# Kernel tuning notes

Measured on AMD Instinct MI355X. Metric: run time of the kernel, lower is better.

## Reference

```python
import jax, jax.numpy as jnp
import numpy as np

L, D, H, KV, HD, KVL, I, PL = 8, 2048, 8, 2, 256, 4096, 8192, 256
FULL = (4,)          # layers with full (global) attention / global RoPE
POS = 2047           # current decode position (cache write slot)
N_REP = H // KV      # GQA expansion factor


def rms(x, eps=1e-6):
    # RMSNorm without scale (v_norm); scale applied by caller where needed
    return x * jax.lax.rsqrt(jnp.mean(x * x, axis=-1, keepdims=True) + eps)


def rope(x, cos, sin):
    half = HD // 2
    rot = jnp.concatenate([-x[..., half:], x[..., :half]], axis=-1)
    return x * cos + rot * sin


def _rope_tables(theta):
    inv = 1.0 / (theta ** (np.arange(0, HD, 2, dtype=np.float32) / HD))
    ang = jnp.asarray(POS * inv, dtype=jnp.float32)
    return jnp.concatenate([jnp.cos(ang)] * 2), jnp.concatenate([jnp.sin(ang)] * 2)


def setup_inputs() -> dict:
    key = jax.random.key(0)
    ks = jax.random.split(key, 24)
    r = lambda k, s, sc=0.02: jax.random.normal(k, s, jnp.float32) * sc
    gains = lambda k, s: 1.0 + jax.random.normal(k, s, jnp.float32) * 0.02
    cos_s, sin_s = _rope_tables(10000.0)
    cos_f, sin_f = _rope_tables(1000000.0)
    um = jnp.zeros((1, 1, KVL, 1), jnp.float32).at[0, 0, POS, 0].set(1.0)
    mask = jnp.where(jnp.arange(KVL) <= POS, 0.0, -1e9).astype(jnp.float32)
    return {
        "hidden_states": r(ks[0], (1, 1, D), 1.0),
        "causal_mask": mask,
        "update_mask": um,
        "per_layer_combined": r(ks[1], (1, 1, L * PL), 1.0),
        "cos_s": cos_s, "sin_s": sin_s, "cos_f": cos_f, "sin_f": sin_f,
        "K_in": r(ks[2], (L, KV, KVL, HD)),
        "V_in": r(ks[3], (L, KV, KVL, HD)),
        "w_q": r(ks[4], (L, H * HD, D)),
        "w_k": r(ks[5], (L, KV * HD, D)),
        "w_v": r(ks[6], (L, KV * HD, D)),
        "w_o": r(ks[7], (L, D, H * HD)),
        "g_in_ln": gains(ks[8], (L, D)),
        "g_q_norm": gains(ks[9], (L, HD)),
        "g_k_norm": gains(ks[10], (L, HD)),
        "g_post_attn_ln": gains(ks[11], (L, D)),
        "g_pre_ff_ln": gains(ks[12], (L, D)),
        "g_post_ff_ln": gains(ks[13], (L, D)),
        "w_gate": r(ks[14], (L, I, D)),
        "w_up": r(ks[15], (L, I, D)),
        "w_down": r(ks[16], (L, D, I)),
        "w_plg": r(ks[17], (L, PL, D)),
        "w_plp": r(ks[18], (L, D, PL)),
        "g_post_pl_ln": gains(ks[19], (L, D)),
        "layer_scalar": jnp.ones((L,), jnp.float32),
    }


def reference(hidden_states, causal_mask, update_mask, per_layer_combined,
              cos_s, sin_s, cos_f, sin_f, K_in, V_in,
              w_q, w_k, w_v, w_o,
              g_in_ln, g_q_norm, g_k_norm, g_post_attn_ln, g_pre_ff_ln, g_post_ff_ln,
              w_gate, w_up, w_down, w_plg, w_plp, g_post_pl_ln, layer_scalar):
    um = update_mask[0, 0]          # [KVL,1] one-hot at write position
    h = hidden_states[0, 0]         # [D], batch=1/seq=1 decode
    K_outs, V_outs = [], []
    for i in range(L):
        cos, sin = (cos_f, sin_f) if i in FULL else (cos_s, sin_s)
        # --- attention block ---
        res = h
        x = rms(h) * g_in_ln[i]
        q = rms((w_q[i] @ x).reshape(H, HD)) * g_q_norm[i]
        q = rope(q, cos, sin)                                   # [H,HD]
        k = rms((w_k[i] @ x).reshape(KV, HD)) * g_k_norm[i]
        k = rope(k, cos, sin)                                   # [KV,HD]
        v = rms((w_v[i] @ x).reshape(KV, HD))                    # v_norm (no scale)
        # full-tensor masked blend = KV cache write (faithful to source)
        Ko = K_in[i] * (1.0 - um) + k[:, None, :] * um          # [KV,KVL,HD]
        Vo = V_in[i] * (1.0 - um) + v[:, None, :] * um
        K_outs.append(Ko); V_outs.append(Vo)
        Ke = jnp.repeat(Ko, N_REP, axis=0)                      # GQA expand [H,KVL,HD]
        Ve = jnp.repeat(Vo, N_REP, axis=0)
        scores = jnp.einsum('hd,hkd->hk', q, Ke) + causal_mask  # no 1/sqrt(hd) in source
        attn = jax.nn.softmax(scores, axis=-1)
        ao = jnp.einsum('hk,hkd->hd', attn, Ve).reshape(H * HD)
        ao = rms(w_o[i] @ ao) * g_post_attn_ln[i]
        h = res + ao
        # --- gated MLP ---
        res = h
        xm = rms(h) * g_pre_ff_ln[i]
        m = w_down[i] @ (jax.nn.gelu(w_gate[i] @ xm, approximate=True) * (w_up[i] @ xm))
        h = res + rms(m) * g_post_ff_ln[i]
        # --- per-layer input gating ---
        res = h
        pls = per_layer_combined[0, 0, i * PL:(i + 1) * PL]     # [PL]
        g = jax.nn.gelu(w_plg[i] @ h, approximate=True) * pls
        h = res + rms(w_plp[i] @ g) * g_post_pl_ln[i]
        h = h * layer_scalar[i]
    return (h[None, None, :], jnp.stack(K_outs), jnp.stack(V_outs))
```

## Files before the change

kernel.cpp:

```cpp
#include <hip/hip_runtime.h>

#define NL   8
#define DIM  2048
#define NH   8
#define NKV  2
#define HD   256
#define KVL  4096
#define FFI  8192
#define PLD  256
#define POS  2047
#define NCH  128
#define CP   16

__device__ __forceinline__ float dot4(float4 a, float4 b){
  return a.x*b.x + a.y*b.y + a.z*b.z + a.w*b.w;
}

__device__ __forceinline__ float waveAllSum(float v){
#pragma unroll
  for(int o=1;o<64;o<<=1) v += __shfl_xor(v,o,64);
  return v;
}

__device__ __forceinline__ float blockSum256(float v, float* red){
  int lane = threadIdx.x & 63, w = threadIdx.x >> 6;
  v = waveAllSum(v);
  __syncthreads();
  if(lane==0) red[w] = v;
  __syncthreads();
  return red[0]+red[1]+red[2]+red[3];
}

__device__ __forceinline__ float gelu_tanh(float v){
  return 0.5f*v*(1.0f + tanhf(0.7978845608028654f*(v + 0.044715f*v*v*v)));
}

__device__ __forceinline__ float4 normRope(const float* __restrict__ raw, int lane,
    const float* __restrict__ gain, const float* __restrict__ cosT,
    const float* __restrict__ sinT, bool doRope){
  float4 v4 = ((const float4*)raw)[lane];
  float ss = waveAllSum(dot4(v4,v4));
  float sc = rsqrtf(ss*(1.f/HD) + 1e-6f);
  float4 n;
  if(gain){
    float4 g4 = ((const float4*)gain)[lane];
    n.x=v4.x*sc*g4.x; n.y=v4.y*sc*g4.y; n.z=v4.z*sc*g4.z; n.w=v4.w*sc*g4.w;
  } else {
    n.x=v4.x*sc; n.y=v4.y*sc; n.z=v4.z*sc; n.w=v4.w*sc;
  }
  if(!doRope) return n;
  float4 np;
  np.x=__shfl_xor(n.x,32,64); np.y=__shfl_xor(n.y,32,64);
  np.z=__shfl_xor(n.z,32,64); np.w=__shfl_xor(n.w,32,64);
  float4 c4 = ((const float4*)cosT)[lane];
  float4 s4 = ((const float4*)sinT)[lane];
  float sg = (lane < 32) ? -1.f : 1.f;
  float4 o;
  o.x = n.x*c4.x + sg*np.x*s4.x;
  o.y = n.y*c4.y + sg*np.y*s4.y;
  o.z = n.z*c4.z + sg*np.z*s4.z;
  o.w = n.w*c4.w + sg*np.w*s4.w;
  return o;
}

__global__ __launch_bounds__(256) void qkv_k(
    const float* __restrict__ Wq, const float* __restrict__ Wk,
    const float* __restrict__ Wv,
    const float* __restrict__ hC, const float* __restrict__ u,
    const float* __restrict__ g_pl, const float* __restrict__ lsc,
    const float* __restrict__ g_in, const float* __restrict__ hidden,
    float* __restrict__ hA, float* __restrict__ qkv){
  __shared__ float xs[DIM];
  __shared__ float red[4];
  int tid = threadIdx.x;
  float hv[8];
  if(hidden){
#pragma unroll
    for(int i=0;i<8;i++) hv[i] = hidden[tid + i*256];
  } else {
    float uv[8]; float ss1 = 0.f;
#pragma unroll
    for(int i=0;i<8;i++){ uv[i] = u[tid + i*256]; ss1 += uv[i]*uv[i]; }
    ss1 = blockSum256(ss1, red);
    float r1 = rsqrtf(ss1*(1.f/DIM) + 1e-6f);
    float ls = lsc[0];
#pragma unroll
    for(int i=0;i<8;i++){
      int idx = tid + i*256;
      hv[i] = (hC[idx] + uv[i]*r1*g_pl[idx])*ls;
    }
  }
  float ss2 = 0.f;
#pragma unroll
  for(int i=0;i<8;i++) ss2 += hv[i]*hv[i];
  ss2 = blockSum256(ss2, red);
  float r2 = rsqrtf(ss2*(1.f/DIM) + 1e-6f);
#pragma unroll
  for(int i=0;i<8;i++){
    int idx = tid + i*256;
    xs[idx] = hv[i]*r2*g_in[idx];
    if(blockIdx.x==0) hA[idx] = hv[i];
  }
  __syncthreads();
  int lane = tid & 63, wv = tid >> 6;
  int r = blockIdx.x*4 + wv;
  const float* W; int row;
  if(r < 2048){ W = Wq; row = r; }
  else if(r < 2560){ W = Wk; row = r - 2048; }
  else { W = Wv; row = r - 2560; }
  const float4* Wr = (const float4*)(W + (size_t)row*DIM);
  const float4* xs4 = (const float4*)xs;
  float4 w8[8];
#pragma unroll
  for(int i=0;i<8;i++) w8[i] = Wr[i*64+lane];
  float acc = 0.f;
#pragma unroll
  for(int i=0;i<8;i++) acc += dot4(w8[i], xs4[i*64+lane]);
  acc = waveAllSum(acc);
  if(lane==0) qkv[r] = acc;
}

__global__ __launch_bounds__(256) void attn_k(
    const float* __restrict__ qkvb,
    const float* __restrict__ gq, const float* __restrict__ gk,
    const float* __restrict__ cosT, const float* __restrict__ sinT,
    float* __restrict__ Kl, float* __restrict__ Vl,
    float* __restrict__ pm, float* __restrict__ pl, float* __restrict__ po){
  int b = blockIdx.x, tid = threadIdx.x, lane = tid & 63, wv = tid >> 6;

  if(b == NKV*NCH){
    int kvv = wv >> 1, isV = wv & 1;
    const float* raw = qkvb + (isV ? 2560 : 2048) + kvv*HD;
    float4 o = normRope(raw, lane, isV ? nullptr : gk, cosT, sinT, !isV);
    float* dst = (isV ? Vl : Kl) + ((size_t)kvv*KVL + POS)*HD;
    ((float4*)dst)[lane] = o;
    return;
  }

  int kv = b & 1, c = b >> 1;
  __shared__ float q_s[4][HD];
  __shared__ float vf_s[HD];
  __shared__ float s_s[4][CP];
  __shared__ float s_w[4][CP];
  bool fresh = (c == NCH-1);

  {
    float4 o = normRope(qkvb + (kv*4 + wv)*HD, lane, gq, cosT, sinT, true);
    ((float4*)q_s[wv])[lane] = o;
  }
  float4 kf4 = {0,0,0,0};
  if(fresh){
    if(wv == 3) kf4 = normRope(qkvb + 2048 + kv*HD, lane, gk, cosT, sinT, true);
    if(wv == 1){
      float4 o = normRope(qkvb + 2560 + kv*HD, lane, nullptr, cosT, sinT, false);
      ((float4*)vf_s)[lane] = o;
    }
  }
  __syncthreads();

  float4 q4[4];
#pragma unroll
  for(int hh=0;hh<4;hh++) q4[hh] = ((const float4*)q_s[hh])[lane];
  const float4* Kp = (const float4*)(Kl + ((size_t)kv*KVL + c*CP)*HD);
#pragma unroll
  for(int j=0;j<4;j++){
    int p = wv*4 + j;
    float4 k4 = (fresh && p==CP-1) ? kf4 : Kp[(size_t)p*64 + lane];
    float d0 = dot4(k4,q4[0]), d1 = dot4(k4,q4[1]);
    float d2 = dot4(k4,q4[2]), d3 = dot4(k4,q4[3]);
    d0 = waveAllSum(d0); d1 = waveAllSum(d1);
    d2 = waveAllSum(d2); d3 = waveAllSum(d3);
    if(lane==0){ s_s[0][p]=d0; s_s[1][p]=d1; s_s[2][p]=d2; s_s[3][p]=d3; }
  }
  __syncthreads();

  if(tid < 64){
    int hh = tid >> 4, pp = tid & 15;
    float s = s_s[hh][pp];
    float m = s;
#pragma unroll
    for(int o=1;o<16;o<<=1) m = fmaxf(m, __shfl_xor(m,o,64));
    float e = __expf(s - m);
    float ls = e;
#pragma unroll
    for(int o=1;o<16;o<<=1) ls += __shfl_xor(ls,o,64);
    s_w[hh][pp] = e;
    if(pp==0){ int hg = kv*4 + hh; pm[hg*NCH + c] = m; pl[hg*NCH + c] = ls; }
  }
  __syncthreads();

  int d = tid;
  const float* Vp = Vl + ((size_t)kv*KVL + c*CP)*HD;
  float vv[CP];
#pragma unroll
  for(int p2=0;p2<CP;p2++) vv[p2] = Vp[(size_t)p2*HD + d];
  if(fresh) vv[CP-1] = vf_s[d];
  float acc[4] = {0.f,0.f,0.f,0.f};
#pragma unroll
  for(int p2=0;p2<CP;p2++){
#pragma unroll
    for(int hh=0;hh<4;hh++) acc[hh] += s_w[hh][p2]*vv[p2];
  }
#pragma unroll
  for(int hh=0;hh<4;hh++)
    po[((size_t)(kv*4+hh)*NCH + c)*HD + d] = acc[hh];
}

__global__ __launch_bounds__(256) void attn_c(const float* __restrict__ pm,
    const float* __restrict__ pl, const float* __restrict__ po, float* __restrict__ ao){
  int h = blockIdx.x, tid = threadIdx.x;
  __shared__ float sm[NCH], sl[NCH], se[NCH];
  if(tid < NCH){ sm[tid] = pm[h*NCH+tid]; sl[tid] = pl[h*NCH+tid]; }
  __syncthreads();
  float M = -1e30f;
  for(int c=0;c<NCH;c++) M = fmaxf(M, sm[c]);
  if(tid < NCH) se[tid] = __expf(sm[tid]-M);
  __syncthreads();
  float Lh = 0.f;
  for(int c=0;c<NCH;c++) Lh += sl[c]*se[c];
  float a0=0.f, a1=0.f, a2=0.f, a3=0.f;
#pragma unroll 1
  for(int c=0;c<NCH;c+=4){
    a0 += po[((size_t)h*NCH + c  )*HD + tid]*se[c];
    a1 += po[((size_t)h*NCH + c+1)*HD + tid]*se[c+1];
    a2 += po[((size_t)h*NCH + c+2)*HD + tid]*se[c+2];
    a3 += po[((size_t)h*NCH + c+3)*HD + tid]*se[c+3];
  }
  ao[h*HD + tid] = (a0+a1+a2+a3) / Lh;
}

template<int C>
__global__ __launch_bounds__(256) void gemv_k(const float* __restrict__ W,
    const float* __restrict__ x, float* __restrict__ y){
  __shared__ float xs[C];
  for(int i=threadIdx.x; i<C/4; i+=256)
    ((float4*)xs)[i] = ((const float4*)x)[i];
  __syncthreads();
  int lane = threadIdx.x & 63, wv = threadIdx.x >> 6;
  int r = blockIdx.x*4 + wv;
  const float4* Wr = (const float4*)(W + (size_t)r*C);
  const float4* xs4 = (const float4*)xs;
  float acc = 0.f;
#pragma unroll
  for(int ii=0;ii<C/2048;ii++){
    float4 w8[8];
#pragma unroll
    for(int i=0;i<8 && ii*8+i < C/256;i++) w8[i] = Wr[(ii*8+i)*64+lane];
#pragma unroll
    for(int i=0;i<8 && ii*8+i < C/256;i++) acc += dot4(w8[i], xs4[(ii*8+i)*64+lane]);
  }
  if(C < 2048){
    float4 w1 = Wr[lane];
    acc = dot4(w1, xs4[lane]);
  }
  acc = waveAllSum(acc);
  if(lane==0) y[r] = acc;
}

__global__ __launch_bounds__(256) void gateup_k(const float* __restrict__ Wg,
    const float* __restrict__ Wu, const float* __restrict__ y,
    const float* __restrict__ hA, const float* __restrict__ g_pa,
    const float* __restrict__ g_pf, float* __restrict__ hB, float* __restrict__ t){
  __shared__ float xs[DIM];
  __shared__ float red[4];
  int tid = threadIdx.x;
  float yv[8]; float ss1 = 0.f;
#pragma unroll
  for(int i=0;i<8;i++){ yv[i] = y[tid + i*256]; ss1 += yv[i]*yv[i]; }
  ss1 = blockSum256(ss1, red);
  float r1 = rsqrtf(ss1*(1.f/DIM) + 1e-6f);
  float hv[8]; float ss2 = 0.f;
#pragma unroll
  for(int i=0;i<8;i++){
    int idx = tid + i*256;
    hv[i] = hA[idx] + yv[i]*r1*g_pa[idx];
    ss2 += hv[i]*hv[i];
  }
  ss2 = blockSum256(ss2, red);
  float r2 = rsqrtf(ss2*(1.f/DIM) + 1e-6f);
#pragma unroll
  for(int i=0;i<8;i++){
    int idx = tid + i*256;
    xs[idx] = hv[i]*r2*g_pf[idx];
    if(blockIdx.x==0) hB[idx] = hv[i];
  }
  __syncthreads();
  int lane = tid & 63, wv = tid >> 6;
  int j = blockIdx.x*4 + wv;
  const float4* Gr = (const float4*)(Wg + (size_t)j*DIM);
  const float4* Ur = (const float4*)(Wu + (size_t)j*DIM);
  const float4* xs4 = (const float4*)xs;
  float4 g8[8], u8[8];
#pragma unroll
  for(int i=0;i<8;i++) g8[i] = Gr[i*64+lane];
#pragma unroll
  for(int i=0;i<8;i++) u8[i] = Ur[i*64+lane];
  float ag = 0.f, au = 0.f;
#pragma unroll
  for(int i=0;i<8;i++){
    float4 bv = xs4[i*64+lane];
    ag += dot4(g8[i], bv);
    au += dot4(u8[i], bv);
  }
  ag = waveAllSum(ag);
  au = waveAllSum(au);
  if(lane==0) t[j] = gelu_tanh(ag)*au;
}

__global__ __launch_bounds__(256) void down_k(const float* __restrict__ Wd,
    const float* __restrict__ t, float* __restrict__ mv){
  __shared__ float red[4];
  int tid = threadIdx.x, lane = tid & 63, wv = tid >> 6;
  int r = blockIdx.x;
  const float4* Wr = (const float4*)(Wd + (size_t)r*FFI) + wv*512;
  const float4* tp = (const float4*)t + wv*512;
  float4 w8[8], t8[8];
#pragma unroll
  for(int i=0;i<8;i++) w8[i] = Wr[i*64+lane];
#pragma unroll
  for(int i=0;i<8;i++) t8[i] = tp[i*64+lane];
  float acc = 0.f;
#pragma unroll
  for(int i=0;i<8;i++) acc += dot4(w8[i], t8[i]);
  acc = waveAllSum(acc);
  if(lane==0) red[wv] = acc;
  __syncthreads();
  if(tid==0) mv[r] = red[0]+red[1]+red[2]+red[3];
}

__global__ __launch_bounds__(256) void plg_k(const float* __restrict__ W,
    const float* __restrict__ mv, const float* __restrict__ hB,
    const float* __restrict__ g_ff, const float* __restrict__ pls,
    float* __restrict__ hCout, float* __restrict__ gb){
  __shared__ float xs[DIM];
  __shared__ float red[4];
  int tid = threadIdx.x;
  float mvv[8]; float ss1 = 0.f;
#pragma unroll
  for(int i=0;i<8;i++){ mvv[i] = mv[tid + i*256]; ss1 += mvv[i]*mvv[i]; }
  ss1 = blockSum256(ss1, red);
  float r1 = rsqrtf(ss1*(1.f/DIM) + 1e-6f);
#pragma unroll
  for(int i=0;i<8;i++){
    int idx = tid + i*256;
    float hc = hB[idx] + mvv[i]*r1*g_ff[idx];
    xs[idx] = hc;
    if(blockIdx.x==0) hCout[idx] = hc;
  }
  __syncthreads();
  int lane = tid & 63, wv = tid >> 6;
  int r = blockIdx.x*4 + wv;
  const float4* Wr = (const float4*)(W + (size_t)r*DIM);
  const float4* xs4 = (const float4*)xs;
  float4 w8[8];
#pragma unroll
  for(int i=0;i<8;i++) w8[i] = Wr[i*64+lane];
  float acc = 0.f;
#pragma unroll
  for(int i=0;i<8;i++) acc += dot4(w8[i], xs4[i*64+lane]);
  acc = waveAllSum(acc);
  if(lane==0) gb[r] = gelu_tanh(acc)*pls[r];
}

__global__ __launch_bounds__(256) void final_k(const float* __restrict__ u,
    const float* __restrict__ hC, const float* __restrict__ g_pl,
    const float* __restrict__ lsc, float* __restrict__ out){
  __shared__ float red[4];
  int tid = threadIdx.x;
  float uv[8]; float ss1 = 0.f;
#pragma unroll
  for(int i=0;i<8;i++){ uv[i] = u[tid + i*256]; ss1 += uv[i]*uv[i]; }
  ss1 = blockSum256(ss1, red);
  float r1 = rsqrtf(ss1*(1.f/DIM) + 1e-6f);
  float ls = lsc[0];
#pragma unroll
  for(int i=0;i<8;i++){
    int idx = tid + i*256;
    out[idx] = (hC[idx] + uv[i]*r1*g_pl[idx])*ls;
  }
}

extern "C" void kernel_launch(void* const* d_in, const int* in_sizes, int n_in,
                              void* d_out, int out_size, void* d_ws, size_t ws_size,
                              hipStream_t stream){
  const float* hidden   = (const float*)d_in[0];
  const float* plc      = (const float*)d_in[3];
  const float* cos_s    = (const float*)d_in[4];
  const float* sin_s    = (const float*)d_in[5];
  const float* cos_f    = (const float*)d_in[6];
  const float* sin_f    = (const float*)d_in[7];
  const float* K_in     = (const float*)d_in[8];
  const float* V_in     = (const float*)d_in[9];
  const float* w_q      = (const float*)d_in[10];
  const float* w_k      = (const float*)d_in[11];
  const float* w_v      = (const float*)d_in[12];
  const float* w_o      = (const float*)d_in[13];
  const float* g_in_ln  = (const float*)d_in[14];
  const float* g_q_norm = (const float*)d_in[15];
  const float* g_k_norm = (const float*)d_in[16];
  const float* g_pa_ln  = (const float*)d_in[17];
  const float* g_pf_ln  = (const float*)d_in[18];
  const float* g_ff_ln  = (const float*)d_in[19];
  const float* w_gate   = (const float*)d_in[20];
  const float* w_up     = (const float*)d_in[21];
  const float* w_down   = (const float*)d_in[22];
  const float* w_plg    = (const float*)d_in[23];
  const float* w_plp    = (const float*)d_in[24];
  const float* g_pl_ln  = (const float*)d_in[25];
  const float* l_scal   = (const float*)d_in[26];

  float* out  = (float*)d_out;
  float* outK = out + DIM;
  float* outV = outK + (size_t)NL*NKV*KVL*HD;

  float* ws   = (float*)d_ws;
  float* hA   = ws;
  float* hB   = ws + 2048;
  float* hC   = ws + 4096;
  float* qkvb = ws + 6144;
  float* y    = ws + 9216;
  float* t    = ws + 11264;
  float* mv   = ws + 19456;
  float* gb   = ws + 21504;
  float* u    = ws + 21760;
  float* pm   = ws + 23808;
  float* pl   = ws + 24832;
  float* po   = ws + 25856;
  float* ao   = ws + 288000;

  (void)hipMemcpyAsync(outK, K_in, (size_t)NL*NKV*KVL*HD*sizeof(float),
                       hipMemcpyDeviceToDevice, stream);
  (void)hipMemcpyAsync(outV, V_in, (size_t)NL*NKV*KVL*HD*sizeof(float),
                       hipMemcpyDeviceToDevice, stream);

  for(int l=0;l<NL;l++){
    const float* cosT = (l==4) ? cos_f : cos_s;
    const float* sinT = (l==4) ? sin_f : sin_s;
    float* Kl = outK + (size_t)l*NKV*KVL*HD;
    float* Vl = outV + (size_t)l*NKV*KVL*HD;

    qkv_k<<<768,256,0,stream>>>(
        w_q + (size_t)l*NH*HD*DIM, w_k + (size_t)l*NKV*HD*DIM,
        w_v + (size_t)l*NKV*HD*DIM,
        hC, u,
        (l>0) ? g_pl_ln + (size_t)(l-1)*DIM : g_pl_ln,
        (l>0) ? l_scal + (l-1) : l_scal,
        g_in_ln + (size_t)l*DIM,
        (l==0) ? hidden : nullptr,
        hA, qkvb);

    attn_k<<<NKV*NCH+1,256,0,stream>>>(qkvb, g_q_norm + l*HD, g_k_norm + l*HD,
                                       cosT, sinT, Kl, Vl, pm, pl, po);

    attn_c<<<NH,256,0,stream>>>(pm, pl, po, ao);

    gemv_k<DIM><<<512,256,0,stream>>>(w_o + (size_t)l*DIM*NH*HD, ao, y);

    gateup_k<<<FFI/4,256,0,stream>>>(w_gate + (size_t)l*FFI*DIM,
                                     w_up + (size_t)l*FFI*DIM,
                                     y, hA, g_pa_ln + (size_t)l*DIM,
                                     g_pf_ln + (size_t)l*DIM, hB, t);

    down_k<<<DIM,256,0,stream>>>(w_down + (size_t)l*DIM*FFI, t, mv);

    plg_k<<<PLD/4,256,0,stream>>>(w_plg + (size_t)l*PLD*DIM, mv, hB,
                                  g_ff_ln + (size_t)l*DIM, plc + l*PLD, hC, gb);

    gemv_k<PLD><<<512,256,0,stream>>>(w_plp + (size_t)l*DIM*PLD, gb, u);
  }

  final_k<<<1,256,0,stream>>>(u, hC, g_pl_ln + (size_t)(NL-1)*DIM,
                              l_scal + (NL-1), out);
}
```

Before: 809.2 us.

## Fuse per-layer kernels into two persistent kernels with atomic-counter stage handoff

Replaces the eight launches per layer with two kernels. Within each kernel, block ranges act as pipeline stages that signal completion and wait on one another through global atomic counters with release and acquire fences. The bulk K/V cache copy moves off the separate memcpy calls and into spare blocks of the attention kernel, using nontemporal loads and stores so it can overlap with compute. Attention now reads the old cache directly from the inputs. The aim is to cut launch gaps and to hide the large cache copy. The cost is reliance on lower-index blocks being scheduled before the blocks that wait on them, which risks deadlock or spin overhead if they are not.

```diff
diff --git a/kernel.cpp b/kernel.cpp
--- a/kernel.cpp
+++ b/kernel.cpp
@@ -12,8 +12,19 @@
 #define NCH  128
 #define CP   16
 
+typedef float vfloat4 __attribute__((ext_vector_type(4)));
+
 __device__ __forceinline__ float dot4(float4 a, float4 b){
   return a.x*b.x + a.y*b.y + a.z*b.z + a.w*b.w;
+}
+
+__device__ __forceinline__ float4 ntld4(const float4* p){
+  vfloat4 v = __builtin_nontemporal_load((const vfloat4*)p);
+  float4 r; r.x=v.x; r.y=v.y; r.z=v.z; r.w=v.w; return r;
+}
+__device__ __forceinline__ void ntst4(float4* p, float4 v){
+  vfloat4 t; t.x=v.x; t.y=v.y; t.z=v.z; t.w=v.w;
+  __builtin_nontemporal_store(t, (vfloat4*)p);
 }
 
 __device__ __forceinline__ float waveAllSum(float v){
@@ -63,320 +74,367 @@
   return o;
 }
 
-__global__ __launch_bounds__(256) void qkv_k(
-    const float* __restrict__ Wq, const float* __restrict__ Wk,
-    const float* __restrict__ Wv,
-    const float* __restrict__ hC, const float* __restrict__ u,
-    const float* __restrict__ g_pl, const float* __restrict__ lsc,
-    const float* __restrict__ g_in, const float* __restrict__ hidden,
-    float* __restrict__ hA, float* __restrict__ qkv){
-  __shared__ float xs[DIM];
+__device__ __forceinline__ void prodSignal(unsigned* c){
+  __syncthreads();
+  if(threadIdx.x == 0){
+    __builtin_amdgcn_fence(__ATOMIC_RELEASE, "agent");
+    __hip_atomic_fetch_add(c, 1u, __ATOMIC_RELAXED, __HIP_MEMORY_SCOPE_AGENT);
+  }
+}
+__device__ __forceinline__ void consWait(unsigned* c, unsigned n){
+  if(threadIdx.x == 0){
+    while(__hip_atomic_load(c, __ATOMIC_RELAXED, __HIP_MEMORY_SCOPE_AGENT) < n)
+      __builtin_amdgcn_s_sleep(2);
+    __builtin_amdgcn_fence(__ATOMIC_ACQUIRE, "agent");
+  }
+  __syncthreads();
+}
+
+__global__ __launch_bounds__(256,4) void init_k(const float* __restrict__ hidden,
+    const float* __restrict__ gin, float* __restrict__ hRes, float* __restrict__ xs){
   __shared__ float red[4];
   int tid = threadIdx.x;
-  float hv[8];
-  if(hidden){
-#pragma unroll
-    for(int i=0;i<8;i++) hv[i] = hidden[tid + i*256];
+  float v[8]; float ss = 0.f;
+#pragma unroll
+  for(int i=0;i<8;i++){ v[i] = hidden[tid + i*256]; ss += v[i]*v[i]; }
+  ss = blockSum256(ss, red);
+  float r = rsqrtf(ss*(1.f/DIM) + 1e-6f);
+#pragma unroll
+  for(int i=0;i<8;i++){ int idx = tid + i*256; hRes[idx] = v[i]; xs[idx] = v[i]*r*gin[idx]; }
+}
+
+__global__ __launch_bounds__(256,4) void ab_k(
+    const float* __restrict__ Wq, const float* __restrict__ Wk,
+    const float* __restrict__ Wv, const float* __restrict__ Wo,
+    const float* __restrict__ Ki, const float* __restrict__ Vi,
+    float* __restrict__ Kl, float* __restrict__ Vl,
+    const float* __restrict__ gq, const float* __restrict__ gk,
+    const float* __restrict__ cosT, const float* __restrict__ sinT,
+    const float* __restrict__ xs, float* __restrict__ qkvb,
+    float* __restrict__ pm, float* __restrict__ pl, float* __restrict__ po,
+    float* __restrict__ ao, float* __restrict__ y,
+    const float* __restrict__ hRes, const float* __restrict__ gpa,
+    const float* __restrict__ gpf, float* __restrict__ hMid, float* __restrict__ xm,
+    unsigned* cnt){
+  __shared__ float sh[2048];
+  __shared__ float red[4];
+  float4* sh4 = (float4*)sh;
+  int b = blockIdx.x, tid = threadIdx.x, lane = tid & 63, wv = tid >> 6;
+  unsigned* c_qkv  = cnt;
+  unsigned* c_attn = cnt + 16;
+  unsigned* c_comb = cnt + 32;
+  unsigned* c_wo   = cnt + 48;
+
+  if(b < 384){
+#pragma unroll
+    for(int i=0;i<2;i++) sh4[tid + i*256] = ((const float4*)xs)[tid + i*256];
+    __syncthreads();
+#pragma unroll
+    for(int rr=0;rr<2;rr++){
+      int r = b*8 + wv*2 + rr;
+      const float* W; int row;
+      if(r < 2048){ W = Wq; row = r; }
+      else if(r < 2560){ W = Wk; row = r - 2048; }
+      else { W = Wv; row = r - 2560; }
+      const float4* Wr = (const float4*)(W + (size_t)row*DIM);
+      float4 w8[8];
+#pragma unroll
+      for(int i=0;i<8;i++) w8[i] = Wr[i*64+lane];
+      float acc = 0.f;
+#pragma unroll
+      for(int i=0;i<8;i++) acc += dot4(w8[i], sh4[i*64+lane]);
+      acc = waveAllSum(acc);
+      if(lane==0) qkvb[r] = acc;
+    }
+    prodSignal(c_qkv);
+  } else if(b < 641){
+    consWait(c_qkv, 384);
+    int b2 = b - 384;
+    if(b2 == 256){
+      int kvv = wv >> 1, isV = wv & 1;
+      const float* raw = qkvb + (isV ? 2560 : 2048) + kvv*HD;
+      float4 o = normRope(raw, lane, isV ? nullptr : gk, cosT, sinT, !isV);
+      float* dst = (isV ? Vl : Kl) + ((size_t)kvv*KVL + POS)*HD;
+      ((float4*)dst)[lane] = o;
+      prodSignal(c_attn);
+      return;
+    }
+    int kv = b2 & 1, c = b2 >> 1;
+    float* q_s  = sh;
+    float* vf_s = sh + 1024;
+    float* s_sB = sh + 1280;
+    float* s_wB = sh + 1344;
+    bool fresh = (c == NCH-1);
+    { float4 o = normRope(qkvb + (kv*4 + wv)*HD, lane, gq, cosT, sinT, true);
+      ((float4*)(q_s + wv*HD))[lane] = o; }
+    float4 kf4 = {0,0,0,0};
+    if(fresh){
+      if(wv == 3) kf4 = normRope(qkvb + 2048 + kv*HD, lane, gk, cosT, sinT, true);
+      if(wv == 1){
+        float4 o = normRope(qkvb + 2560 + kv*HD, lane, nullptr, cosT, sinT, false);
+        ((float4*)vf_s)[lane] = o;
+      }
+    }
+    __syncthreads();
+    float4 q4[4];
+#pragma unroll
+    for(int hh=0;hh<4;hh++) q4[hh] = ((const float4*)(q_s + hh*HD))[lane];
+    const float4* Kp = (const float4*)(Ki + ((size_t)kv*KVL + c*CP)*HD);
+#pragma unroll
+    for(int j=0;j<4;j++){
+      int p = wv*4 + j;
+      float4 k4 = (fresh && p==CP-1) ? kf4 : Kp[(size_t)p*64 + lane];
+      float d0 = dot4(k4,q4[0]), d1 = dot4(k4,q4[1]);
+      float d2 = dot4(k4,q4[2]), d3 = dot4(k4,q4[3]);
+      d0 = waveAllSum(d0); d1 = waveAllSum(d1);
+      d2 = waveAllSum(d2); d3 = waveAllSum(d3);
+      if(lane==0){ s_sB[0*CP+p]=d0; s_sB[1*CP+p]=d1; s_sB[2*CP+p]=d2; s_sB[3*CP+p]=d3; }
+    }
+    __syncthreads();
+    if(tid < 64){
+      int hh = tid >> 4, pp = tid & 15;
+      float s = s_sB[hh*CP+pp];
+      float m = s;
+#pragma unroll
+      for(int o=1;o<16;o<<=1) m = fmaxf(m, __shfl_xor(m,o,64));
+      float e = __expf(s - m);
+      float ls = e;
+#pragma unroll
+      for(int o=1;o<16;o<<=1) ls += __shfl_xor(ls,o,64);
+      s_wB[hh*CP+pp] = e;
+      if(pp==0){ int hg = kv*4 + hh; pm[hg*NCH + c] = m; pl[hg*NCH + c] = ls; }
+    }
+    __syncthreads();
+    int d = tid;
+    const float* Vp = Vi + ((size_t)kv*KVL + c*CP)*HD;
+    float vv[CP];
+#pragma unroll
+    for(int p2=0;p2<CP;p2++) vv[p2] = Vp[(size_t)p2*HD + d];
+    if(fresh) vv[CP-1] = vf_s[d];
+    float acc[4] = {0.f,0.f,0.f,0.f};
+#pragma unroll
+    for(int p2=0;p2<CP;p2++){
+#pragma unroll
+      for(int hh=0;hh<4;hh++) acc[hh] += s_wB[hh*CP+p2]*vv[p2];
+    }
+#pragma unroll
+    for(int hh=0;hh<4;hh++)
+      po[((size_t)(kv*4+hh)*NCH + c)*HD + d] = acc[hh];
+    prodSignal(c_attn);
+  } else if(b < 649){
+    consWait(c_attn, 257);
+    int h = b - 641;
+    float* sm = sh; float* sl = sh + 128; float* se = sh + 256;
+    if(tid < NCH){ sm[tid] = pm[h*NCH+tid]; sl[tid] = pl[h*NCH+tid]; }
+    __syncthreads();
+    float M = -1e30f;
+    for(int c=0;c<NCH;c++) M = fmaxf(M, sm[c]);
+    if(tid < NCH) se[tid] = __expf(sm[tid]-M);
+    __syncthreads();
+    float Lh = 0.f;
+    for(int c=0;c<NCH;c++) Lh += sl[c]*se[c];
+    float a0=0.f,a1=0.f,a2=0.f,a3=0.f;
+#pragma unroll 1
+    for(int c=0;c<NCH;c+=4){
+      a0 += po[((size_t)h*NCH + c  )*HD + tid]*se[c];
+      a1 += po[((size_t)h*NCH + c+1)*HD + tid]*se[c+1];
+      a2 += po[((size_t)h*NCH + c+2)*HD + tid]*se[c+2];
+      a3 += po[((size_t)h*NCH + c+3)*HD + tid]*se[c+3];
+    }
+    ao[h*HD + tid] = (a0+a1+a2+a3) / Lh;
+    prodSignal(c_comb);
+  } else if(b < 777){
+    consWait(c_comb, 8);
+    int b4 = b - 649;
+#pragma unroll
+    for(int i=0;i<2;i++) sh4[tid + i*256] = ((const float4*)ao)[tid + i*256];
+    __syncthreads();
+#pragma unroll
+    for(int j=0;j<4;j++){
+      int r = b4*16 + wv*4 + j;
+      const float4* Wr = (const float4*)(Wo + (size_t)r*DIM);
+      float4 w8[8];
+#pragma unroll
+      for(int i=0;i<8;i++) w8[i] = Wr[i*64+lane];
+      float acc = 0.f;
+#pragma unroll
+      for(int i=0;i<8;i++) acc += dot4(w8[i], sh4[i*64+lane]);
+      acc = waveAllSum(acc);
+      if(lane==0) y[r] = acc;
+    }
+    prodSignal(c_wo);
+  } else if(b == 777){
+    consWait(c_wo, 128);
+    float yv[8]; float ss1 = 0.f;
+#pragma unroll
+    for(int i=0;i<8;i++){ yv[i] = y[tid + i*256]; ss1 += yv[i]*yv[i]; }
+    ss1 = blockSum256(ss1, red);
+    float r1 = rsqrtf(ss1*(1.f/DIM) + 1e-6f);
+    float hv[8]; float ss2 = 0.f;
+#pragma unroll
+    for(int i=0;i<8;i++){
+      int idx = tid + i*256;
+      hv[i] = hRes[idx] + yv[i]*r1*gpa[idx];
+      ss2 += hv[i]*hv[i];
+    }
+    ss2 = blockSum256(ss2, red);
+    float r2 = rsqrtf(ss2*(1.f/DIM) + 1e-6f);
+#pragma unroll
+    for(int i=0;i<8;i++){
+      int idx = tid + i*256;
+      hMid[idx] = hv[i];
+      xm[idx] = hv[i]*r2*gpf[idx];
+    }
   } else {
+    int b5 = b - 778;
+#pragma unroll 4
+    for(int i=0;i<32;i++){
+      int gr = b5*128 + wv*32 + i;
+      int pos = gr & 4095;
+      if(pos == POS) continue;
+      const float4* s; float4* dpt;
+      if(gr < 8192){ s = (const float4*)Ki + (size_t)gr*64; dpt = (float4*)Kl + (size_t)gr*64; }
+      else { int g2 = gr - 8192; s = (const float4*)Vi + (size_t)g2*64; dpt = (float4*)Vl + (size_t)g2*64; }
+      ntst4(dpt + lane, ntld4(s + lane));
+    }
+  }
+}
+
+__global__ __launch_bounds__(256,4) void cde_k(
+    const float* __restrict__ Wg, const float* __restrict__ Wu,
+    const float* __restrict__ Wd, const float* __restrict__ Wpg,
+    const float* __restrict__ Wpp,
+    const float* __restrict__ xm, float* __restrict__ t, float* __restrict__ mv,
+    const float* __restrict__ hMid, const float* __restrict__ gff,
+    const float* __restrict__ pls, float* __restrict__ hFF, float* __restrict__ gb,
+    float* __restrict__ u,
+    const float* __restrict__ gpl, const float* __restrict__ lsc,
+    const float* __restrict__ ginN, float* __restrict__ hRes, float* __restrict__ xs,
+    float* __restrict__ outv,
+    unsigned* cnt){
+  __shared__ float sh[8192];
+  __shared__ float red[4];
+  float4* sh4 = (float4*)sh;
+  int b = blockIdx.x, tid = threadIdx.x, lane = tid & 63, wv = tid >> 6;
+  unsigned* c_gu   = cnt + 64;
+  unsigned* c_down = cnt + 80;
+  unsigned* c_plg  = cnt + 96;
+  unsigned* c_plp  = cnt + 112;
+
+  if(b < 256){
+#pragma unroll
+    for(int i=0;i<2;i++) sh4[tid + i*256] = ((const float4*)xm)[tid + i*256];
+    __syncthreads();
+#pragma unroll 1
+    for(int jj=0;jj<8;jj++){
+      int j = b*32 + wv*8 + jj;
+      const float4* Gr = (const float4*)(Wg + (size_t)j*DIM);
+      const float4* Ur = (const float4*)(Wu + (size_t)j*DIM);
+      float4 g8[8], u8[8];
+#pragma unroll
+      for(int i=0;i<8;i++) g8[i] = Gr[i*64+lane];
+#pragma unroll
+      for(int i=0;i<8;i++) u8[i] = Ur[i*64+lane];
+      float ag = 0.f, au = 0.f;
+#pragma unroll
+      for(int i=0;i<8;i++){
+        float4 bv = sh4[i*64+lane];
+        ag += dot4(g8[i], bv);
+        au += dot4(u8[i], bv);
+      }
+      ag = waveAllSum(ag);
+      au = waveAllSum(au);
+      if(lane==0) t[j] = gelu_tanh(ag)*au;
+    }
+    prodSignal(c_gu);
+  } else if(b < 768){
+    consWait(c_gu, 256);
+#pragma unroll
+    for(int i=0;i<8;i++) sh4[tid + i*256] = ((const float4*)t)[tid + i*256];
+    __syncthreads();
+    int r = (b-256)*4 + wv;
+    const float4* Wr = (const float4*)(Wd + (size_t)r*FFI);
+    float acc = 0.f;
+#pragma unroll 1
+    for(int bb=0;bb<4;bb++){
+      float4 w8[8];
+#pragma unroll
+      for(int i=0;i<8;i++) w8[i] = Wr[(bb*8+i)*64+lane];
+#pragma unroll
+      for(int i=0;i<8;i++) acc += dot4(w8[i], sh4[(bb*8+i)*64+lane]);
+    }
+    acc = waveAllSum(acc);
+    if(lane==0) mv[r] = acc;
+    prodSignal(c_down);
+  } else if(b < 832){
+    consWait(c_down, 512);
+    float mvv[8]; float ss1 = 0.f;
+#pragma unroll
+    for(int i=0;i<8;i++){ mvv[i] = mv[tid + i*256]; ss1 += mvv[i]*mvv[i]; }
+    ss1 = blockSum256(ss1, red);
+    float r1 = rsqrtf(ss1*(1.f/DIM) + 1e-6f);
+#pragma unroll
+    for(int i=0;i<8;i++){
+      int idx = tid + i*256;
+      float hc = hMid[idx] + mvv[i]*r1*gff[idx];
+      sh[idx] = hc;
+      if(b==768) hFF[idx] = hc;
+    }
+    __syncthreads();
+    int r = (b-768)*4 + wv;
+    const float4* Wr = (const float4*)(Wpg + (size_t)r*DIM);
+    float4 w8[8];
+#pragma unroll
+    for(int i=0;i<8;i++) w8[i] = Wr[i*64+lane];
+    float acc = 0.f;
+#pragma unroll
+    for(int i=0;i<8;i++) acc += dot4(w8[i], sh4[i*64+lane]);
+    acc = waveAllSum(acc);
+    if(lane==0) gb[r] = gelu_tanh(acc)*pls[r];
+    prodSignal(c_plg);
+  } else if(b < 960){
+    consWait(c_plg, 64);
+    if(tid < 64) sh4[tid] = ((const float4*)gb)[tid];
+    __syncthreads();
+#pragma unroll
+    for(int j=0;j<4;j++){
+      int r = (b-832)*16 + wv*4 + j;
+      const float4* Wr = (const float4*)(Wpp + (size_t)r*PLD);
+      float acc = dot4(Wr[lane], sh4[lane]);
+      acc = waveAllSum(acc);
+      if(lane==0) u[r] = acc;
+    }
+    prodSignal(c_plp);
+  } else {
+    consWait(c_plp, 128);
     float uv[8]; float ss1 = 0.f;
 #pragma unroll
     for(int i=0;i<8;i++){ uv[i] = u[tid + i*256]; ss1 += uv[i]*uv[i]; }
     ss1 = blockSum256(ss1, red);
     float r1 = rsqrtf(ss1*(1.f/DIM) + 1e-6f);
     float ls = lsc[0];
+    float h3[8];
 #pragma unroll
     for(int i=0;i<8;i++){
       int idx = tid + i*256;
-      hv[i] = (hC[idx] + uv[i]*r1*g_pl[idx])*ls;
-    }
-  }
-  float ss2 = 0.f;
-#pragma unroll
-  for(int i=0;i<8;i++) ss2 += hv[i]*hv[i];
-  ss2 = blockSum256(ss2, red);
-  float r2 = rsqrtf(ss2*(1.f/DIM) + 1e-6f);
-#pragma unroll
-  for(int i=0;i<8;i++){
-    int idx = tid + i*256;
-    xs[idx] = hv[i]*r2*g_in[idx];
-    if(blockIdx.x==0) hA[idx] = hv[i];
-  }
-  __syncthreads();
-  int lane = tid & 63, wv = tid >> 6;
-  int r = blockIdx.x*4 + wv;
-  const float* W; int row;
-  if(r < 2048){ W = Wq; row = r; }
-  else if(r < 2560){ W = Wk; row = r - 2048; }
-  else { W = Wv; row = r - 2560; }
-  const float4* Wr = (const float4*)(W + (size_t)row*DIM);
-  const float4* xs4 = (const float4*)xs;
-  float4 w8[8];
-#pragma unroll
-  for(int i=0;i<8;i++) w8[i] = Wr[i*64+lane];
-  float acc = 0.f;
-#pragma unroll
-  for(int i=0;i<8;i++) acc += dot4(w8[i], xs4[i*64+lane]);
-  acc = waveAllSum(acc);
-  if(lane==0) qkv[r] = acc;
-}
-
-__global__ __launch_bounds__(256) void attn_k(
-    const float* __restrict__ qkvb,
-    const float* __restrict__ gq, const float* __restrict__ gk,
-    const float* __restrict__ cosT, const float* __restrict__ sinT,
-    float* __restrict__ Kl, float* __restrict__ Vl,
-    float* __restrict__ pm, float* __restrict__ pl, float* __restrict__ po){
-  int b = blockIdx.x, tid = threadIdx.x, lane = tid & 63, wv = tid >> 6;
-
-  if(b == NKV*NCH){
-    int kvv = wv >> 1, isV = wv & 1;
-    const float* raw = qkvb + (isV ? 2560 : 2048) + kvv*HD;
-    float4 o = normRope(raw, lane, isV ? nullptr : gk, cosT, sinT, !isV);
-    float* dst = (isV ? Vl : Kl) + ((size_t)kvv*KVL + POS)*HD;
-    ((float4*)dst)[lane] = o;
-    return;
-  }
-
-  int kv = b & 1, c = b >> 1;
-  __shared__ float q_s[4][HD];
-  __shared__ float vf_s[HD];
-  __shared__ float s_s[4][CP];
-  __shared__ float s_w[4][CP];
-  bool fresh = (c == NCH-1);
-
-  {
-    float4 o = normRope(qkvb + (kv*4 + wv)*HD, lane, gq, cosT, sinT, true);
-    ((float4*)q_s[wv])[lane] = o;
-  }
-  float4 kf4 = {0,0,0,0};
-  if(fresh){
-    if(wv == 3) kf4 = normRope(qkvb + 2048 + kv*HD, lane, gk, cosT, sinT, true);
-    if(wv == 1){
-      float4 o = normRope(qkvb + 2560 + kv*HD, lane, nullptr, cosT, sinT, false);
-      ((float4*)vf_s)[lane] = o;
-    }
-  }
-  __syncthreads();
-
-  float4 q4[4];
-#pragma unroll
-  for(int hh=0;hh<4;hh++) q4[hh] = ((const float4*)q_s[hh])[lane];
-  const float4* Kp = (const float4*)(Kl + ((size_t)kv*KVL + c*CP)*HD);
-#pragma unroll
-  for(int j=0;j<4;j++){
-    int p = wv*4 + j;
-    float4 k4 = (fresh && p==CP-1) ? kf4 : Kp[(size_t)p*64 + lane];
-    float d0 = dot4(k4,q4[0]), d1 = dot4(k4,q4[1]);
-    float d2 = dot4(k4,q4[2]), d3 = dot4(k4,q4[3]);
-    d0 = waveAllSum(d0); d1 = waveAllSum(d1);
-    d2 = waveAllSum(d2); d3 = waveAllSum(d3);
-    if(lane==0){ s_s[0][p]=d0; s_s[1][p]=d1; s_s[2][p]=d2; s_s[3][p]=d3; }
-  }
-  __syncthreads();
-
-  if(tid < 64){
-    int hh = tid >> 4, pp = tid & 15;
-    float s = s_s[hh][pp];
-    float m = s;
-#pragma unroll
-    for(int o=1;o<16;o<<=1) m = fmaxf(m, __shfl_xor(m,o,64));
-    float e = __expf(s - m);
-    float ls = e;
-#pragma unroll
-    for(int o=1;o<16;o<<=1) ls += __shfl_xor(ls,o,64);
-    s_w[hh][pp] = e;
-    if(pp==0){ int hg = kv*4 + hh; pm[hg*NCH + c] = m; pl[hg*NCH + c] = ls; }
-  }
-  __syncthreads();
-
-  int d = tid;
-  const float* Vp = Vl + ((size_t)kv*KVL + c*CP)*HD;
-  float vv[CP];
-#pragma unroll
-  for(int p2=0;p2<CP;p2++) vv[p2] = Vp[(size_t)p2*HD + d];
-  if(fresh) vv[CP-1] = vf_s[d];
-  float acc[4] = {0.f,0.f,0.f,0.f};
-#pragma unroll
-  for(int p2=0;p2<CP;p2++){
-#pragma unroll
-    for(int hh=0;hh<4;hh++) acc[hh] += s_w[hh][p2]*vv[p2];
-  }
-#pragma unroll
-  for(int hh=0;hh<4;hh++)
-    po[((size_t)(kv*4+hh)*NCH + c)*HD + d] = acc[hh];
-}
-
-__global__ __launch_bounds__(256) void attn_c(const float* __restrict__ pm,
-    const float* __restrict__ pl, const float* __restrict__ po, float* __restrict__ ao){
-  int h = blockIdx.x, tid = threadIdx.x;
-  __shared__ float sm[NCH], sl[NCH], se[NCH];
-  if(tid < NCH){ sm[tid] = pm[h*NCH+tid]; sl[tid] = pl[h*NCH+tid]; }
-  __syncthreads();
-  float M = -1e30f;
-  for(int c=0;c<NCH;c++) M = fmaxf(M, sm[c]);
-  if(tid < NCH) se[tid] = __expf(sm[tid]-M);
-  __syncthreads();
-  float Lh = 0.f;
-  for(int c=0;c<NCH;c++) Lh += sl[c]*se[c];
-  float a0=0.f, a1=0.f, a2=0.f, a3=0.f;
-#pragma unroll 1
-  for(int c=0;c<NCH;c+=4){
-    a0 += po[((size_t)h*NCH + c  )*HD + tid]*se[c];
-    a1 += po[((size_t)h*NCH + c+1)*HD + tid]*se[c+1];
-    a2 += po[((size_t)h*NCH + c+2)*HD + tid]*se[c+2];
-    a3 += po[((size_t)h*NCH + c+3)*HD + tid]*se[c+3];
-  }
-  ao[h*HD + tid] = (a0+a1+a2+a3) / Lh;
-}
-
-template<int C>
-__global__ __launch_bounds__(256) void gemv_k(const float* __restrict__ W,
-    const float* __restrict__ x, float* __restrict__ y){
-  __shared__ float xs[C];
-  for(int i=threadIdx.x; i<C/4; i+=256)
-    ((float4*)xs)[i] = ((const float4*)x)[i];
-  __syncthreads();
-  int lane = threadIdx.x & 63, wv = threadIdx.x >> 6;
-  int r = blockIdx.x*4 + wv;
-  const float4* Wr = (const float4*)(W + (size_t)r*C);
-  const float4* xs4 = (const float4*)xs;
-  float acc = 0.f;
-#pragma unroll
-  for(int ii=0;ii<C/2048;ii++){
-    float4 w8[8];
-#pragma unroll
-    for(int i=0;i<8 && ii*8+i < C/256;i++) w8[i] = Wr[(ii*8+i)*64+lane];
-#pragma unroll
-    for(int i=0;i<8 && ii*8+i < C/256;i++) acc += dot4(w8[i], xs4[(ii*8+i)*64+lane]);
-  }
-  if(C < 2048){
-    float4 w1 = Wr[lane];
-    acc = dot4(w1, xs4[lane]);
-  }
-  acc = waveAllSum(acc);
-  if(lane==0) y[r] = acc;
-}
-
-__global__ __launch_bounds__(256) void gateup_k(const float* __restrict__ Wg,
-    const float* __restrict__ Wu, const float* __restrict__ y,
-    const float* __restrict__ hA, const float* __restrict__ g_pa,
-    const float* __restrict__ g_pf, float* __restrict__ hB, float* __restrict__ t){
-  __shared__ float xs[DIM];
-  __shared__ float red[4];
-  int tid = threadIdx.x;
-  float yv[8]; float ss1 = 0.f;
-#pragma unroll
-  for(int i=0;i<8;i++){ yv[i] = y[tid + i*256]; ss1 += yv[i]*yv[i]; }
-  ss1 = blockSum256(ss1, red);
-  float r1 = rsqrtf(ss1*(1.f/DIM) + 1e-6f);
-  float hv[8]; float ss2 = 0.f;
-#pragma unroll
-  for(int i=0;i<8;i++){
-    int idx = tid + i*256;
-    hv[i] = hA[idx] + yv[i]*r1*g_pa[idx];
-    ss2 += hv[i]*hv[i];
-  }
-  ss2 = blockSum256(ss2, red);
-  float r2 = rsqrtf(ss2*(1.f/DIM) + 1e-6f);
-#pragma unroll
-  for(int i=0;i<8;i++){
-    int idx = tid + i*256;
-    xs[idx] = hv[i]*r2*g_pf[idx];
-    if(blockIdx.x==0) hB[idx] = hv[i];
-  }
-  __syncthreads();
-  int lane = tid & 63, wv = tid >> 6;
-  int j = blockIdx.x*4 + wv;
-  const float4* Gr = (const float4*)(Wg + (size_t)j*DIM);
-  const float4* Ur = (const float4*)(Wu + (size_t)j*DIM);
-  const float4* xs4 = (const float4*)xs;
-  float4 g8[8], u8[8];
-#pragma unroll
-  for(int i=0;i<8;i++) g8[i] = Gr[i*64+lane];
-#pragma unroll
-  for(int i=0;i<8;i++) u8[i] = Ur[i*64+lane];
-  float ag = 0.f, au = 0.f;
-#pragma unroll
-  for(int i=0;i<8;i++){
-    float4 bv = xs4[i*64+lane];
-    ag += dot4(g8[i], bv);
-    au += dot4(u8[i], bv);
-  }
-  ag = waveAllSum(ag);
-  au = waveAllSum(au);
-  if(lane==0) t[j] = gelu_tanh(ag)*au;
-}
-
-__global__ __launch_bounds__(256) void down_k(const float* __restrict__ Wd,
-    const float* __restrict__ t, float* __restrict__ mv){
-  __shared__ float red[4];
-  int tid = threadIdx.x, lane = tid & 63, wv = tid >> 6;
-  int r = blockIdx.x;
-  const float4* Wr = (const float4*)(Wd + (size_t)r*FFI) + wv*512;
-  const float4* tp = (const float4*)t + wv*512;
-  float4 w8[8], t8[8];
-#pragma unroll
-  for(int i=0;i<8;i++) w8[i] = Wr[i*64+lane];
-#pragma unroll
-  for(int i=0;i<8;i++) t8[i] = tp[i*64+lane];
-  float acc = 0.f;
-#pragma unroll
-  for(int i=0;i<8;i++) acc += dot4(w8[i], t8[i]);
-  acc = waveAllSum(acc);
-  if(lane==0) red[wv] = acc;
-  __syncthreads();
-  if(tid==0) mv[r] = red[0]+red[1]+red[2]+red[3];
-}
-
-__global__ __launch_bounds__(256) void plg_k(const float* __restrict__ W,
-    const float* __restrict__ mv, const float* __restrict__ hB,
-    const float* __restrict__ g_ff, const float* __restrict__ pls,
-    float* __restrict__ hCout, float* __restrict__ gb){
-  __shared__ float xs[DIM];
-  __shared__ float red[4];
-  int tid = threadIdx.x;
-  float mvv[8]; float ss1 = 0.f;
-#pragma unroll
-  for(int i=0;i<8;i++){ mvv[i] = mv[tid + i*256]; ss1 += mvv[i]*mvv[i]; }
-  ss1 = blockSum256(ss1, red);
-  float r1 = rsqrtf(ss1*(1.f/DIM) + 1e-6f);
-#pragma unroll
-  for(int i=0;i<8;i++){
-    int idx = tid + i*256;
-    float hc = hB[idx] + mvv[i]*r1*g_ff[idx];
-    xs[idx] = hc;
-    if(blockIdx.x==0) hCout[idx] = hc;
-  }
-  __syncthreads();
-  int lane = tid & 63, wv = tid >> 6;
-  int r = blockIdx.x*4 + wv;
-  const float4* Wr = (const float4*)(W + (size_t)r*DIM);
-  const float4* xs4 = (const float4*)xs;
-  float4 w8[8];
-#pragma unroll
-  for(int i=0;i<8;i++) w8[i] = Wr[i*64+lane];
-  float acc = 0.f;
-#pragma unroll
-  for(int i=0;i<8;i++) acc += dot4(w8[i], xs4[i*64+lane]);
-  acc = waveAllSum(acc);
-  if(lane==0) gb[r] = gelu_tanh(acc)*pls[r];
-}
-
-__global__ __launch_bounds__(256) void final_k(const float* __restrict__ u,
-    const float* __restrict__ hC, const float* __restrict__ g_pl,
-    const float* __restrict__ lsc, float* __restrict__ out){
-  __shared__ float red[4];
-  int tid = threadIdx.x;
-  float uv[8]; float ss1 = 0.f;
-#pragma unroll
-  for(int i=0;i<8;i++){ uv[i] = u[tid + i*256]; ss1 += uv[i]*uv[i]; }
-  ss1 = blockSum256(ss1, red);
-  float r1 = rsqrtf(ss1*(1.f/DIM) + 1e-6f);
-  float ls = lsc[0];
-#pragma unroll
-  for(int i=0;i<8;i++){
-    int idx = tid + i*256;
-    out[idx] = (hC[idx] + uv[i]*r1*g_pl[idx])*ls;
+      h3[i] = (hFF[idx] + uv[i]*r1*gpl[idx])*ls;
+    }
+    if(outv){
+#pragma unroll
+      for(int i=0;i<8;i++) outv[tid + i*256] = h3[i];
+    } else {
+      float ss2 = 0.f;
+#pragma unroll
+      for(int i=0;i<8;i++) ss2 += h3[i]*h3[i];
+      ss2 = blockSum256(ss2, red);
+      float r2 = rsqrtf(ss2*(1.f/DIM) + 1e-6f);
+#pragma unroll
+      for(int i=0;i<8;i++){
+        int idx = tid + i*256;
+        hRes[idx] = h3[i];
+        xs[idx] = h3[i]*r2*ginN[idx];
+      }
+    }
   }
 }
 
@@ -413,62 +471,55 @@
   float* outK = out + DIM;
   float* outV = outK + (size_t)NL*NKV*KVL*HD;
 
-  float* ws   = (float*)d_ws;
-  float* hA   = ws;
-  float* hB   = ws + 2048;
-  float* hC   = ws + 4096;
-  float* qkvb = ws + 6144;
-  float* y    = ws + 9216;
-  float* t    = ws + 11264;
-  float* mv   = ws + 19456;
-  float* gb   = ws + 21504;
-  float* u    = ws + 21760;
-  float* pm   = ws + 23808;
-  float* pl   = ws + 24832;
-  float* po   = ws + 25856;
-  float* ao   = ws + 288000;
-
-  (void)hipMemcpyAsync(outK, K_in, (size_t)NL*NKV*KVL*HD*sizeof(float),
-                       hipMemcpyDeviceToDevice, stream);
-  (void)hipMemcpyAsync(outV, V_in, (size_t)NL*NKV*KVL*HD*sizeof(float),
-                       hipMemcpyDeviceToDevice, stream);
+  unsigned* cnt = (unsigned*)d_ws;
+
+  float* fws  = (float*)d_ws + 1024;
+  float* hRes = fws;
+  float* hMid = fws + 2048;
+  float* hFF  = fws + 4096;
+  float* xs   = fws + 6144;
+  float* xm   = fws + 8192;
+  float* qkvb = fws + 10240;
+  float* y    = fws + 13312;
+  float* t    = fws + 15360;
+  float* mv   = fws + 23552;
+  float* gb   = fws + 25600;
+  float* u    = fws + 25856;
+  float* pm   = fws + 27904;
+  float* pl   = fws + 28928;
+  float* ao   = fws + 29952;
+  float* po   = fws + 32000;
+
+  (void)hipMemsetAsync(d_ws, 0, 4096, stream);
+  init_k<<<1,256,0,stream>>>(hidden, g_in_ln, hRes, xs);
 
   for(int l=0;l<NL;l++){
     const float* cosT = (l==4) ? cos_f : cos_s;
     const float* sinT = (l==4) ? sin_f : sin_s;
     float* Kl = outK + (size_t)l*NKV*KVL*HD;
     float* Vl = outV + (size_t)l*NKV*KVL*HD;
-
-    qkv_k<<<768,256,0,stream>>>(
+    const float* Ki = K_in + (size_t)l*NKV*KVL*HD;
+    const float* Vi = V_in + (size_t)l*NKV*KVL*HD;
+    unsigned* lc = cnt + l*128;
+
+    ab_k<<<906,256,0,stream>>>(
         w_q + (size_t)l*NH*HD*DIM, w_k + (size_t)l*NKV*HD*DIM,
-        w_v + (size_t)l*NKV*HD*DIM,
-        hC, u,
-        (l>0) ? g_pl_ln + (size_t)(l-1)*DIM : g_pl_ln,
-        (l>0) ? l_scal + (l-1) : l_scal,
-        g_in_ln + (size_t)l*DIM,
-        (l==0) ? hidden : nullptr,
-        hA, qkvb);
-
-    attn_k<<<NKV*NCH+1,256,0,stream>>>(qkvb, g_q_norm + l*HD, g_k_norm + l*HD,
-                                       cosT, sinT, Kl, Vl, pm, pl, po);
-
-    attn_c<<<NH,256,0,stream>>>(pm, pl, po, ao);
-
-    gemv_k<DIM><<<512,256,0,stream>>>(w_o + (size_t)l*DIM*NH*HD, ao, y);
-
-    gateup_k<<<FFI/4,256,0,stream>>>(w_gate + (size_t)l*FFI*DIM,
-                                     w_up + (size_t)l*FFI*DIM,
-                                     y, hA, g_pa_ln + (size_t)l*DIM,
-                                     g_pf_ln + (size_t)l*DIM, hB, t);
-
-    down_k<<<DIM,256,0,stream>>>(w_down + (size_t)l*DIM*FFI, t, mv);
-
-    plg_k<<<PLD/4,256,0,stream>>>(w_plg + (size_t)l*PLD*DIM, mv, hB,
-                                  g_ff_ln + (size_t)l*DIM, plc + l*PLD, hC, gb);
-
-    gemv_k<PLD><<<512,256,0,stream>>>(w_plp + (size_t)l*DIM*PLD, gb, u);
+        w_v + (size_t)l*NKV*HD*DIM, w_o + (size_t)l*DIM*NH*HD,
+        Ki, Vi, Kl, Vl,
+        g_q_norm + l*HD, g_k_norm + l*HD, cosT, sinT,
+        xs, qkvb, pm, pl, po, ao, y,
+        hRes, g_pa_ln + (size_t)l*DIM, g_pf_ln + (size_t)l*DIM, hMid, xm,
+        lc);
+
+    cde_k<<<961,256,0,stream>>>(
+        w_gate + (size_t)l*FFI*DIM, w_up + (size_t)l*FFI*DIM,
+        w_down + (size_t)l*DIM*FFI, w_plg + (size_t)l*PLD*DIM,
+        w_plp + (size_t)l*DIM*PLD,
+        xm, t, mv,
+        hMid, g_ff_ln + (size_t)l*DIM, plc + l*PLD, hFF, gb, u,
+        g_pl_ln + (size_t)l*DIM, l_scal + l,
+        g_in_ln + (size_t)((l+1)%NL)*DIM, hRes, xs,
+        (l==NL-1) ? out : nullptr,
+        lc);
   }
-
-  final_k<<<1,256,0,stream>>>(u, hC, g_pl_ln + (size_t)(NL-1)*DIM,
-                              l_scal + (NL-1), out);
-}
+}
```

New measurement: 1.753 ms. 2.17x slower.
